# Kernel optimization log

Hardware: AMD Instinct MI355X
Metric: run time of the kernel (lower is better)

## Reference

```python
import jax, jax.numpy as jnp
import numpy as np

NUM_ITERATIONS = 3  # dynamic routing iterations
EPS = 1e-8
IN_LEN = 8   # capsule length after conv (out_length of CapsuleConv2d)
OUT_LEN = 16
OUT_CAPS = 10


def squash(s, axis=-1):
    # v = (|s|^2 / (1+|s|^2)) * s/|s|
    n2 = jnp.sum(s * s, axis=axis, keepdims=True)
    return (n2 / (1.0 + n2)) * s * jax.lax.rsqrt(n2 + EPS)


def setup_inputs() -> dict:
    key = jax.random.key(0)
    k1, k2, k3 = jax.random.split(key, 3)
    B = 16384
    x = jax.random.normal(k1, (B, 1, 3, 3), dtype=jnp.float32)
    # CapsuleConv2d weight: standard conv kernel [out_ch, in_ch, k, k]
    conv_w = 0.1 * jax.random.normal(k2, (32, 1, 3, 3), dtype=jnp.float32)
    # CapsuleLinear routing weight: [out_capsules, in_capsules, out_length, in_length]
    lin_w = 0.1 * jax.random.normal(k3, (OUT_CAPS, 36, OUT_LEN, IN_LEN), dtype=jnp.float32)
    return {"x": x, "conv_w": conv_w, "lin_w": lin_w}


def reference(x, conv_w, lin_w):
    B = x.shape[0]
    # --- CapsuleConv2d: conv2d (stride 1, pad 1) + squash over capsule length ---
    y = jax.lax.conv_general_dilated(
        x, conv_w, window_strides=(1, 1), padding=((1, 1), (1, 1)),
        dimension_numbers=("NCHW", "OIHW", "NCHW"))  # [B,32,3,3]
    H, W = y.shape[2], y.shape[3]
    G = y.shape[1] // IN_LEN  # 4 capsule groups of 8 channels
    y = y.reshape(B, G, IN_LEN, H, W)
    y = squash(y, axis=2)
    # capsules per spatial location: [B, H*W*G, in_length] = [B,36,8]
    caps = y.transpose(0, 3, 4, 1, 2).reshape(B, H * W * G, IN_LEN)

    # --- CapsuleLinear: priors + dynamic routing by agreement ---
    # priors[b,o,i,d] = sum_l lin_w[o,i,d,l] * caps[b,i,l]
    priors = jnp.einsum("oidl,bil->boid", lin_w, caps)  # [B,10,36,16]
    logits = jnp.zeros(priors.shape[:3] + (1,), dtype=priors.dtype)  # [B,10,36,1]
    out = None
    for it in range(NUM_ITERATIONS):
        probs = jax.nn.softmax(logits, axis=1)            # coupling over out_capsules
        out = squash(jnp.sum(probs * priors, axis=2))      # [B,10,16]
        if it != NUM_ITERATIONS - 1:
            # agreement: priors . out
            logits = logits + jnp.sum(priors * out[:, :, None, :], axis=-1, keepdims=True)
    return out  # [B,10,16]
```

## Files before the change

### kernel.cpp

```cpp
#include <hip/hip_runtime.h>

constexpr int OC = 10, NI = 36, OD = 16, IL = 8;
constexpr int M_BLK   = 16;
constexpr int M_INNER = 2;
constexpr int NGROUPS = M_BLK / M_INNER;
constexpr int NT      = 768;
constexpr int SROW    = 18;
constexpr int SPL_SZ  = OC * NI * SROW;

__global__ __launch_bounds__(NT, 1)
void capsnet_kernel(const float* __restrict__ xg,
                    const float* __restrict__ cwg,
                    const float* __restrict__ lwg,
                    float* __restrict__ outg) {
    __shared__ float xs[M_BLK * 9];
    __shared__ float cw[288];
    __shared__ float caps_t[IL * M_BLK * NI];
    __shared__ float spl[M_INNER * SPL_SZ];
    __shared__ float el[M_INNER * NI * OC];
    __shared__ float sinv[M_INNER * NI];
    __shared__ float outl[M_INNER * OC * OD];

    const int t  = threadIdx.x;
    const int b0 = blockIdx.x * M_BLK;

    if (t < M_BLK * 9) xs[t] = xg[b0 * 9 + t];
    if (t < 288)       cw[t] = cwg[t];

    const bool act = t < 2 * OC * NI;
    const int o  = t / (2 * NI);
    const int i  = (t % (2 * NI)) >> 1;
    const int dh = t & 1;

    float4 w4[16];
    if (act) {
        const float4* wp = reinterpret_cast<const float4*>(
            lwg + ((o * NI + i) * OD + dh * 8) * IL);
        #pragma unroll
        for (int j = 0; j < 16; ++j) w4[j] = wp[j];
    }
    __syncthreads();

    for (int task = t; task < M_BLK * NI; task += NT) {
        const int m  = task / NI;
        const int ci = task % NI;
        const int cg = ci & 3;
        const int wx = (ci >> 2) % 3;
        const int hx = ci / 12;
        float acc[IL] = {0.f,0.f,0.f,0.f,0.f,0.f,0.f,0.f};
        #pragma unroll
        for (int kh = 0; kh < 3; ++kh) {
            const int xh = hx + kh - 1;
            if (xh < 0 || xh > 2) continue;
            #pragma unroll
            for (int kw = 0; kw < 3; ++kw) {
                const int xw = wx + kw - 1;
                if (xw < 0 || xw > 2) continue;
                const float xv = xs[m * 9 + xh * 3 + xw];
                #pragma unroll
                for (int l = 0; l < IL; ++l)
                    acc[l] += xv * cw[(cg * 8 + l) * 9 + kh * 3 + kw];
            }
        }
        float n2 = 0.f;
        #pragma unroll
        for (int l = 0; l < IL; ++l) n2 += acc[l] * acc[l];
        const float sc = n2 / (1.f + n2) * rsqrtf(n2 + 1e-8f);
        #pragma unroll
        for (int l = 0; l < IL; ++l)
            caps_t[l * (M_BLK * NI) + task] = acc[l] * sc;
    }
    __syncthreads();

    for (int grp = 0; grp < NGROUPS; ++grp) {
        float P[M_INNER][8];
        float lg[M_INNER];
        float p[M_INNER];
        float ee[M_INNER];
        if (act) {
            #pragma unroll
            for (int m = 0; m < M_INNER; ++m) {
                float cc[IL];
                #pragma unroll
                for (int l = 0; l < IL; ++l)
                    cc[l] = caps_t[l * (M_BLK * NI) + (grp * M_INNER + m) * NI + i];
                #pragma unroll
                for (int d = 0; d < 8; ++d) {
                    const float4 a  = w4[d * 2];
                    const float4 b4 = w4[d * 2 + 1];
                    P[m][d] = a.x  * cc[0] + a.y  * cc[1] + a.z  * cc[2] + a.w  * cc[3]
                            + b4.x * cc[4] + b4.y * cc[5] + b4.z * cc[6] + b4.w * cc[7];
                }
                lg[m] = 0.f;
            }
        }
        p[0] = 0.1f; p[1] = 0.1f;

        for (int it = 0; it < 3; ++it) {
            if (act) {
                #pragma unroll
                for (int m = 0; m < M_INNER; ++m) {
                    float* row = &spl[m * SPL_SZ + (o * NI + i) * SROW + dh * 8];
                    #pragma unroll
                    for (int d = 0; d < 8; d += 2) {
                        float2 v = make_float2(p[m] * P[m][d], p[m] * P[m][d + 1]);
                        *reinterpret_cast<float2*>(row + d) = v;
                    }
                }
            }
            __syncthreads();
            if (t < M_INNER * OC * OD) {
                const int m  = t / (OC * OD);
                const int od = t % (OC * OD);
                const int oo = od / OD;
                const int d  = od % OD;
                const float* col = &spl[m * SPL_SZ + oo * NI * SROW + d];
                float s = 0.f;
                #pragma unroll
                for (int ii = 0; ii < NI; ++ii) s += col[ii * SROW];
                float n2 = s * s;
                n2 += __shfl_xor(n2, 1, 16);
                n2 += __shfl_xor(n2, 2, 16);
                n2 += __shfl_xor(n2, 4, 16);
                n2 += __shfl_xor(n2, 8, 16);
                const float sc = n2 / (1.f + n2) * rsqrtf(n2 + 1e-8f);
                const float ov = s * sc;
                if (it == 2) outg[(b0 + grp * M_INNER + m) * (OC * OD) + od] = ov;
                else         outl[m * (OC * OD) + od] = ov;
            }
            __syncthreads();
            if (it == 2) break;
            if (act) {
                #pragma unroll
                for (int m = 0; m < M_INNER; ++m) {
                    const float* om = &outl[m * (OC * OD) + o * OD + dh * 8];
                    float dpart = 0.f;
                    #pragma unroll
                    for (int d = 0; d < 8; ++d) dpart += P[m][d] * om[d];
                    const float delta = dpart + __shfl_xor(dpart, 1);
                    lg[m] += delta;
                    ee[m] = __expf(lg[m]);
                    if (dh == 0) el[m * (NI * OC) + i * OC + o] = ee[m];
                }
            }
            __syncthreads();
            if (t < M_INNER * NI) {
                const float* er = &el[(t / NI) * (NI * OC) + (t % NI) * OC];
                float ss = 0.f;
                #pragma unroll
                for (int o2 = 0; o2 < OC; ++o2) ss += er[o2];
                sinv[t] = 1.f / ss;
            }
            __syncthreads();
            if (act) {
                p[0] = ee[0] * sinv[i];
                p[1] = ee[1] * sinv[NI + i];
            }
        }
    }
}

extern "C" void kernel_launch(void* const* d_in, const int* in_sizes, int n_in,
                              void* d_out, int out_size, void* d_ws, size_t ws_size,
                              hipStream_t stream) {
    const float* x  = (const float*)d_in[0];
    const float* cw = (const float*)d_in[1];
    const float* lw = (const float*)d_in[2];
    float* out = (float*)d_out;
    const int B = in_sizes[0] / 9;
    dim3 grid(B / M_BLK), block(NT);
    capsnet_kernel<<<grid, block, 0, stream>>>(x, cw, lw, out);
}
```

Before: 224.9 us.

## Store priors once per group and apply routing probs in the reduction

Priors are now written to shared memory once per batch group instead of being rescaled by the coupling probability and rewritten every routing iteration. The reduction threads apply the softmax probabilities from a new normalized-probability table and sum float4 columns with a small shuffle reduction. Two samples per group become four, halving group-loop barriers, and caps storage becomes row-major with float4 access. Shared memory use grows and the reduction phase uses fewer threads, each doing more work.

```diff
diff --git a/kernel.cpp b/kernel.cpp
--- a/kernel.cpp
+++ b/kernel.cpp
@@ -2,11 +2,12 @@
 
 constexpr int OC = 10, NI = 36, OD = 16, IL = 8;
 constexpr int M_BLK   = 16;
-constexpr int M_INNER = 2;
+constexpr int M_INNER = 4;
 constexpr int NGROUPS = M_BLK / M_INNER;
 constexpr int NT      = 768;
-constexpr int SROW    = 18;
-constexpr int SPL_SZ  = OC * NI * SROW;
+constexpr int SROW = 20;
+constexpr int CROW = 12;
+constexpr int PROW = 37;
 
 __global__ __launch_bounds__(NT, 1)
 void capsnet_kernel(const float* __restrict__ xg,
@@ -15,10 +16,10 @@
                     float* __restrict__ outg) {
     __shared__ float xs[M_BLK * 9];
     __shared__ float cw[288];
-    __shared__ float caps_t[IL * M_BLK * NI];
-    __shared__ float spl[M_INNER * SPL_SZ];
+    __shared__ float caps_s[M_BLK * NI * CROW];
+    __shared__ float spl[M_INNER * OC * NI * SROW];
     __shared__ float el[M_INNER * NI * OC];
-    __shared__ float sinv[M_INNER * NI];
+    __shared__ float ptab[M_INNER * OC * PROW];
     __shared__ float outl[M_INNER * OC * OD];
 
     const int t  = threadIdx.x;
@@ -28,9 +29,10 @@
     if (t < 288)       cw[t] = cwg[t];
 
     const bool act = t < 2 * OC * NI;
-    const int o  = t / (2 * NI);
-    const int i  = (t % (2 * NI)) >> 1;
-    const int dh = t & 1;
+    const int o  = t / 72;
+    const int r  = t % 72;
+    const int i  = r >> 1;
+    const int dh = r & 1;
 
     float4 w4[16];
     if (act) {
@@ -41,9 +43,9 @@
     }
     __syncthreads();
 
-    for (int task = t; task < M_BLK * NI; task += NT) {
-        const int m  = task / NI;
-        const int ci = task % NI;
+    if (t < M_BLK * NI) {
+        const int m  = t / NI;
+        const int ci = t % NI;
         const int cg = ci & 3;
         const int wx = (ci >> 2) % 3;
         const int hx = ci / 12;
@@ -66,96 +68,105 @@
         #pragma unroll
         for (int l = 0; l < IL; ++l) n2 += acc[l] * acc[l];
         const float sc = n2 / (1.f + n2) * rsqrtf(n2 + 1e-8f);
-        #pragma unroll
-        for (int l = 0; l < IL; ++l)
-            caps_t[l * (M_BLK * NI) + task] = acc[l] * sc;
+        float4* cp = reinterpret_cast<float4*>(caps_s + (m * NI + ci) * CROW);
+        cp[0] = make_float4(acc[0]*sc, acc[1]*sc, acc[2]*sc, acc[3]*sc);
+        cp[1] = make_float4(acc[4]*sc, acc[5]*sc, acc[6]*sc, acc[7]*sc);
     }
     __syncthreads();
 
     for (int grp = 0; grp < NGROUPS; ++grp) {
         float P[M_INNER][8];
         float lg[M_INNER];
-        float p[M_INNER];
-        float ee[M_INNER];
         if (act) {
             #pragma unroll
             for (int m = 0; m < M_INNER; ++m) {
-                float cc[IL];
-                #pragma unroll
-                for (int l = 0; l < IL; ++l)
-                    cc[l] = caps_t[l * (M_BLK * NI) + (grp * M_INNER + m) * NI + i];
+                const float4* cp = reinterpret_cast<const float4*>(
+                    caps_s + ((grp * M_INNER + m) * NI + i) * CROW);
+                const float4 c0 = cp[0], c1 = cp[1];
                 #pragma unroll
                 for (int d = 0; d < 8; ++d) {
-                    const float4 a  = w4[d * 2];
-                    const float4 b4 = w4[d * 2 + 1];
-                    P[m][d] = a.x  * cc[0] + a.y  * cc[1] + a.z  * cc[2] + a.w  * cc[3]
-                            + b4.x * cc[4] + b4.y * cc[5] + b4.z * cc[6] + b4.w * cc[7];
+                    const float4 a  = w4[2*d], b4 = w4[2*d + 1];
+                    P[m][d] = a.x*c0.x + a.y*c0.y + a.z*c0.z + a.w*c0.w
+                            + b4.x*c1.x + b4.y*c1.y + b4.z*c1.z + b4.w*c1.w;
                 }
+                float4* sp = reinterpret_cast<float4*>(
+                    spl + ((m * OC + o) * NI + i) * SROW + dh * 8);
+                sp[0] = make_float4(P[m][0], P[m][1], P[m][2], P[m][3]);
+                sp[1] = make_float4(P[m][4], P[m][5], P[m][6], P[m][7]);
                 lg[m] = 0.f;
             }
         }
-        p[0] = 0.1f; p[1] = 0.1f;
+        __syncthreads();
 
         for (int it = 0; it < 3; ++it) {
+            if (t < M_INNER * OC * 4) {
+                const int rm = t / 40;
+                const int rr = t % 40;
+                const int ro = rr >> 2;
+                const int dq = rr & 3;
+                const float4* base = reinterpret_cast<const float4*>(
+                    spl + (rm * OC + ro) * NI * SROW) + dq;
+                float4 s4 = make_float4(0.f, 0.f, 0.f, 0.f);
+                if (it == 0) {
+                    #pragma unroll
+                    for (int ii = 0; ii < NI; ++ii) {
+                        const float4 v = base[ii * 5];
+                        s4.x += v.x; s4.y += v.y; s4.z += v.z; s4.w += v.w;
+                    }
+                    s4.x *= 0.1f; s4.y *= 0.1f; s4.z *= 0.1f; s4.w *= 0.1f;
+                } else {
+                    const float* pr = ptab + (rm * OC + ro) * PROW;
+                    #pragma unroll
+                    for (int ii = 0; ii < NI; ++ii) {
+                        const float pv = pr[ii];
+                        const float4 v = base[ii * 5];
+                        s4.x += pv * v.x; s4.y += pv * v.y;
+                        s4.z += pv * v.z; s4.w += pv * v.w;
+                    }
+                }
+                float n2 = s4.x*s4.x + s4.y*s4.y + s4.z*s4.z + s4.w*s4.w;
+                n2 += __shfl_xor(n2, 1);
+                n2 += __shfl_xor(n2, 2);
+                const float sc = n2 / (1.f + n2) * rsqrtf(n2 + 1e-8f);
+                const float4 ov = make_float4(s4.x*sc, s4.y*sc, s4.z*sc, s4.w*sc);
+                if (it == 2)
+                    *reinterpret_cast<float4*>(
+                        outg + (b0 + grp * M_INNER + rm) * (OC * OD) + ro * OD + dq * 4) = ov;
+                else
+                    *reinterpret_cast<float4*>(
+                        outl + rm * (OC * OD) + ro * OD + dq * 4) = ov;
+            }
+            __syncthreads();
+            if (it == 2) break;
+
             if (act) {
                 #pragma unroll
                 for (int m = 0; m < M_INNER; ++m) {
-                    float* row = &spl[m * SPL_SZ + (o * NI + i) * SROW + dh * 8];
-                    #pragma unroll
-                    for (int d = 0; d < 8; d += 2) {
-                        float2 v = make_float2(p[m] * P[m][d], p[m] * P[m][d + 1]);
-                        *reinterpret_cast<float2*>(row + d) = v;
-                    }
+                    const float4* omp = reinterpret_cast<const float4*>(
+                        outl + m * (OC * OD) + o * OD + dh * 8);
+                    const float4 oa = omp[0], ob = omp[1];
+                    float dp = P[m][0]*oa.x + P[m][1]*oa.y + P[m][2]*oa.z + P[m][3]*oa.w
+                             + P[m][4]*ob.x + P[m][5]*ob.y + P[m][6]*ob.z + P[m][7]*ob.w;
+                    dp += __shfl_xor(dp, 1);
+                    lg[m] += dp;
+                    if (dh == 0) el[(m * NI + i) * OC + o] = __expf(lg[m]);
                 }
             }
             __syncthreads();
-            if (t < M_INNER * OC * OD) {
-                const int m  = t / (OC * OD);
-                const int od = t % (OC * OD);
-                const int oo = od / OD;
-                const int d  = od % OD;
-                const float* col = &spl[m * SPL_SZ + oo * NI * SROW + d];
-                float s = 0.f;
-                #pragma unroll
-                for (int ii = 0; ii < NI; ++ii) s += col[ii * SROW];
-                float n2 = s * s;
-                n2 += __shfl_xor(n2, 1, 16);
-                n2 += __shfl_xor(n2, 2, 16);
-                n2 += __shfl_xor(n2, 4, 16);
-                n2 += __shfl_xor(n2, 8, 16);
-                const float sc = n2 / (1.f + n2) * rsqrtf(n2 + 1e-8f);
-                const float ov = s * sc;
-                if (it == 2) outg[(b0 + grp * M_INNER + m) * (OC * OD) + od] = ov;
-                else         outl[m * (OC * OD) + od] = ov;
-            }
-            __syncthreads();
-            if (it == 2) break;
-            if (act) {
-                #pragma unroll
-                for (int m = 0; m < M_INNER; ++m) {
-                    const float* om = &outl[m * (OC * OD) + o * OD + dh * 8];
-                    float dpart = 0.f;
-                    #pragma unroll
-                    for (int d = 0; d < 8; ++d) dpart += P[m][d] * om[d];
-                    const float delta = dpart + __shfl_xor(dpart, 1);
-                    lg[m] += delta;
-                    ee[m] = __expf(lg[m]);
-                    if (dh == 0) el[m * (NI * OC) + i * OC + o] = ee[m];
-                }
-            }
-            __syncthreads();
+
             if (t < M_INNER * NI) {
-                const float* er = &el[(t / NI) * (NI * OC) + (t % NI) * OC];
+                const int em = t / NI;
+                const int ei = t % NI;
+                const float* er = el + (em * NI + ei) * OC;
                 float ss = 0.f;
                 #pragma unroll
                 for (int o2 = 0; o2 < OC; ++o2) ss += er[o2];
-                sinv[t] = 1.f / ss;
+                const float inv = 1.f / ss;
+                #pragma unroll
+                for (int o2 = 0; o2 < OC; ++o2)
+                    ptab[(em * OC + o2) * PROW + ei] = er[o2] * inv;
             }
             __syncthreads();
-            if (act) {
-                p[0] = ee[0] * sinv[i];
-                p[1] = ee[1] * sinv[NI + i];
-            }
         }
     }
 }
@@ -164,10 +175,10 @@
                               void* d_out, int out_size, void* d_ws, size_t ws_size,
                               hipStream_t stream) {
     const float* x  = (const float*)d_in[0];
-    const float* cw = (const float*)d_in[1];
+    const float* cwp = (const float*)d_in[1];
     const float* lw = (const float*)d_in[2];
     float* out = (float*)d_out;
     const int B = in_sizes[0] / 9;
     dim3 grid(B / M_BLK), block(NT);
-    capsnet_kernel<<<grid, block, 0, stream>>>(x, cw, lw, out);
+    capsnet_kernel<<<grid, block, 0, stream>>>(x, cwp, lw, out);
 }
```

New measurement: 453.2 us. 2.01x slower.
